# Kernel tuning notes

Hardware: AMD Instinct MI355X
Metric: run time of the kernel (lower is better)

Reference implementation:

```python
import jax, jax.numpy as jnp
import numpy as np

INPUT_DIM = 1024
OUT_DIM = 1024
ORDER = 4
EXPANSION_POINT = 0.0


def setup_inputs() -> dict:
    key = jax.random.key(0)
    k_x, k_c = jax.random.split(key)
    x = jax.random.normal(k_x, (8192, INPUT_DIM), dtype=jnp.float32)
    coeffs = jax.random.normal(k_c, (OUT_DIM, INPUT_DIM, ORDER), dtype=jnp.float32) * 0.01
    bias = jnp.zeros((1, OUT_DIM), dtype=jnp.float32)
    return {"x": x, "coeffs": coeffs, "bias": bias}


def reference(x, coeffs, bias):
    # x: [..., input_dim] -> flatten leading dims
    outshape = x.shape[:-1] + (OUT_DIM,)
    xf = x.reshape(-1, INPUT_DIM)
    x_shifted = xf - EXPANSION_POINT
    # powers P[n, i, k] = x_shifted^k, k = 0..order-1 (0**0 == 1, matching torch)
    powers = jnp.power(x_shifted[:, :, None], jnp.arange(ORDER, dtype=x.dtype))
    # y[n, o] = sum_{i,k} P[n,i,k] * coeffs[o,i,k]  -- single GEMM-like contraction
    y = jnp.einsum('nik,oik->no', powers, coeffs)
    y = y + bias
    return y.reshape(outshape)
```

## Files before the change

### kernel.cpp

```cpp
#include <hip/hip_runtime.h>
#include <stdint.h>

#define IN_DIM 1024
#define OUT_DIM 1024
#define NROWS 8192
#define KD 3072

#define BM 128
#define BN 128
#define BK 64
#define NT (KD / BK)

typedef __bf16 bf16x8 __attribute__((ext_vector_type(8)));
typedef float f32x4 __attribute__((ext_vector_type(4)));
typedef unsigned short us8 __attribute__((ext_vector_type(8)));
typedef unsigned int u32;

#define AS1 __attribute__((address_space(1)))
#define AS3 __attribute__((address_space(3)))

__device__ __forceinline__ unsigned short f2bf(float f) {
    u32 u = __builtin_bit_cast(u32, f);
    u32 r = (u + 0x7fffu + ((u >> 16) & 1u)) >> 16;
    return (unsigned short)r;
}

__device__ __forceinline__ bf16x8 ld8(const unsigned short* p) {
    return __builtin_bit_cast(bf16x8, *reinterpret_cast<const us8*>(p));
}

__global__ __launch_bounds__(256) void prep_coeffs(const float* __restrict__ c,
                                                   const float* __restrict__ bias,
                                                   unsigned short* __restrict__ B,
                                                   float* __restrict__ bias2) {
    const int o = blockIdx.x;
    const float4* row = reinterpret_cast<const float4*>(c + (size_t)o * (IN_DIM * 4));
    unsigned short* Bo = B + (size_t)o * KD;
    float s = 0.f;
    for (int i = threadIdx.x; i < IN_DIM; i += 256) {
        float4 v = row[i];
        s += v.x;
        Bo[i]        = f2bf(v.y);
        Bo[1024 + i] = f2bf(v.z);
        Bo[2048 + i] = f2bf(v.w);
    }
#pragma unroll
    for (int off = 32; off; off >>= 1) s += __shfl_down(s, off);
    __shared__ float red[4];
    if ((threadIdx.x & 63) == 0) red[threadIdx.x >> 6] = s;
    __syncthreads();
    if (threadIdx.x == 0) bias2[o] = bias[o] + red[0] + red[1] + red[2] + red[3];
}

__global__ __launch_bounds__(256) void prep_powers(const float* __restrict__ x,
                                                   unsigned short* __restrict__ A) {
    int t = blockIdx.x * blockDim.x + threadIdx.x;
    int n = t >> 8;
    int i4 = (t & 255) * 4;
    float4 v = reinterpret_cast<const float4*>(x)[t];
    unsigned short* An = A + (size_t)n * KD + i4;
    float xs[4] = {v.x, v.y, v.z, v.w};
    unsigned short b1[4], b2[4], b3[4];
#pragma unroll
    for (int j = 0; j < 4; ++j) {
        float x1 = xs[j], x2 = x1 * x1, x3 = x2 * x1;
        b1[j] = f2bf(x1); b2[j] = f2bf(x2); b3[j] = f2bf(x3);
    }
    ushort4 p1 = {b1[0], b1[1], b1[2], b1[3]};
    ushort4 p2 = {b2[0], b2[1], b2[2], b2[3]};
    ushort4 p3 = {b3[0], b3[1], b3[2], b3[3]};
    *reinterpret_cast<ushort4*>(An)        = p1;
    *reinterpret_cast<ushort4*>(An + 1024) = p2;
    *reinterpret_cast<ushort4*>(An + 2048) = p3;
}

__global__ __launch_bounds__(256, 2) void taylor_gemm(
    const unsigned short* __restrict__ A,
    const unsigned short* __restrict__ B,
    const float* __restrict__ bias2,
    float* __restrict__ C) {
    __shared__ alignas(16) unsigned short sA[2][BM * BK];
    __shared__ alignas(16) unsigned short sB[2][BN * BK];

    const int tid = threadIdx.x;
    const int lane = tid & 63;
    const int wid = tid >> 6;
    const int wr = wid >> 1;
    const int wc = wid & 1;
    const int gx = blockIdx.x, gy = blockIdx.y;

    const char* Ab = (const char*)A;
    const char* Bb = (const char*)B;
    const int cs = ((lane & 7) ^ (lane >> 3)) * 8;
    size_t aSrc[4], bSrc[4];
    int dstOff[4];
#pragma unroll
    for (int u = 0; u < 4; ++u) {
        int row = u * 32 + wid * 8 + (lane >> 3);
        aSrc[u] = ((size_t)(gx * BM + row) * KD + cs) * 2;
        bSrc[u] = ((size_t)(gy * BN + row) * KD + cs) * 2;
        dstOff[u] = row * BK - (lane >> 3) * BK;
    }

    auto stage_all = [&](int d, int kt) {
        size_t koff = (size_t)kt * (BK * 2);
#pragma unroll
        for (int u = 0; u < 4; ++u)
            __builtin_amdgcn_global_load_lds(
                (const AS1 void*)(Ab + aSrc[u] + koff),
                (AS3 void*)(&sA[d][dstOff[u]]), 16, 0, 0);
#pragma unroll
        for (int u = 0; u < 4; ++u)
            __builtin_amdgcn_global_load_lds(
                (const AS1 void*)(Bb + bSrc[u] + koff),
                (AS3 void*)(&sB[d][dstOff[u]]), 16, 0, 0);
    };

    int aSw[2], bSw[2];
#pragma unroll
    for (int ks = 0; ks < 2; ++ks) {
        int sw = ((ks * 4 + (lane >> 4)) ^ (lane & 7)) * 8;
        aSw[ks] = (wr * 64 + (lane & 15)) * BK + sw;
        bSw[ks] = (wc * 64 + (lane & 15)) * BK + sw;
    }

    f32x4 acc[4][4] = {};

    stage_all(0, 0);
    asm volatile("s_waitcnt vmcnt(0)" ::: "memory");
    __builtin_amdgcn_s_barrier();
    __builtin_amdgcn_sched_barrier(0);

    for (int kt = 0; kt < NT; ++kt) {
        const int d = kt & 1;
        const unsigned short* sAc = &sA[d][0];
        const unsigned short* sBc = &sB[d][0];

        bf16x8 af[4][2], bf[4][2];
#pragma unroll
        for (int m = 0; m < 4; ++m)
#pragma unroll
            for (int ks = 0; ks < 2; ++ks)
                af[m][ks] = ld8(&sAc[aSw[ks] + m * 16 * BK]);
#pragma unroll
        for (int n = 0; n < 4; ++n)
#pragma unroll
            for (int ks = 0; ks < 2; ++ks)
                bf[n][ks] = ld8(&sBc[bSw[ks] + n * 16 * BK]);

        if (kt + 1 < NT) stage_all(d ^ 1, kt + 1);

#pragma unroll
        for (int m = 0; m < 4; ++m)
#pragma unroll
            for (int n = 0; n < 4; ++n)
#pragma unroll
                for (int ks = 0; ks < 2; ++ks)
                    acc[m][n] = __builtin_amdgcn_mfma_f32_16x16x32_bf16(
                        af[m][ks], bf[n][ks], acc[m][n], 0, 0, 0);

        asm volatile("s_waitcnt vmcnt(0)" ::: "memory");
        __builtin_amdgcn_s_barrier();
        __builtin_amdgcn_sched_barrier(0);
    }

    const int colBase = gy * BN + wc * 64 + (lane & 15);
    const int rowBase = gx * BM + wr * 64 + (lane >> 4) * 4;
#pragma unroll
    for (int n = 0; n < 4; ++n) {
        int col = colBase + n * 16;
        float bv = bias2[col];
#pragma unroll
        for (int m = 0; m < 4; ++m) {
            int row = rowBase + m * 16;
#pragma unroll
            for (int r = 0; r < 4; ++r)
                C[(size_t)(row + r) * OUT_DIM + col] = acc[m][n][r] + bv;
        }
    }
}

__global__ void taylor_naive(const float* __restrict__ x, const float* __restrict__ coeffs,
                             const float* __restrict__ bias, float* __restrict__ out) {
    int n = blockIdx.x;
    __shared__ float P[IN_DIM * 4];
    for (int i = threadIdx.x; i < IN_DIM; i += blockDim.x) {
        float xv = x[(size_t)n * IN_DIM + i];
        P[i * 4 + 0] = 1.f;
        P[i * 4 + 1] = xv;
        P[i * 4 + 2] = xv * xv;
        P[i * 4 + 3] = xv * xv * xv;
    }
    __syncthreads();
    for (int o = threadIdx.x; o < OUT_DIM; o += blockDim.x) {
        float s = bias[o];
        const float* c = coeffs + (size_t)o * (IN_DIM * 4);
        for (int i = 0; i < IN_DIM; ++i) {
            float4 cv = *reinterpret_cast<const float4*>(c + i * 4);
            s += cv.x * P[i * 4 + 0] + cv.y * P[i * 4 + 1] +
                 cv.z * P[i * 4 + 2] + cv.w * P[i * 4 + 3];
        }
        out[(size_t)n * OUT_DIM + o] = s;
    }
}

extern "C" void kernel_launch(void* const* d_in, const int* in_sizes, int n_in,
                              void* d_out, int out_size, void* d_ws, size_t ws_size,
                              hipStream_t stream) {
    const float* x = (const float*)d_in[0];
    const float* coeffs = (const float*)d_in[1];
    const float* bias = (const float*)d_in[2];
    float* out = (float*)d_out;

    const size_t needA = (size_t)NROWS * KD * 2;
    const size_t needB = (size_t)OUT_DIM * KD * 2;
    const size_t needBias = OUT_DIM * sizeof(float);

    if (ws_size >= needA + needB + needBias) {
        unsigned short* A = (unsigned short*)d_ws;
        unsigned short* B = (unsigned short*)((char*)d_ws + needA);
        float* bias2 = (float*)((char*)d_ws + needA + needB);
        prep_coeffs<<<OUT_DIM, 256, 0, stream>>>(coeffs, bias, B, bias2);
        prep_powers<<<(NROWS * IN_DIM / 4) / 256, 256, 0, stream>>>(x, A);
        dim3 grid(NROWS / BM, OUT_DIM / BN);
        taylor_gemm<<<grid, 256, 0, stream>>>(A, B, bias2, out);
    } else {
        taylor_naive<<<NROWS, 256, 0, stream>>>(x, coeffs, bias, out);
    }
}
```

Measured before the change: 76.86 us.

## Load A fragments straight from global into double-buffered registers, keep B in LDS

The GEMM now skips LDS staging for the A (powers) operand. Each wave reads its A MFMA fragments directly from global memory into two register buffers that alternate between k-steps, while B is still staged into double-buffered LDS through global_load_lds. The full vmcnt(0) wait is relaxed to vmcnt(8), so the next k-tile's A loads can stay in flight while the current tile's MFMAs run. This removes LDS writes and reads for A and halves LDS use. In exchange, the two waves sharing the same rows fetch the same A data twice, the per-lane global reads are strided, and register pressure rises.

New measurement: 134.4 us. +74.9%, slower.

```diff
diff --git a/kernel.cpp b/kernel.cpp
--- a/kernel.cpp
+++ b/kernel.cpp
@@ -79,7 +79,6 @@
     const unsigned short* __restrict__ B,
     const float* __restrict__ bias2,
     float* __restrict__ C) {
-    __shared__ alignas(16) unsigned short sA[2][BM * BK];
     __shared__ alignas(16) unsigned short sB[2][BN * BK];
 
     const int tid = threadIdx.x;
@@ -89,26 +88,19 @@
     const int wc = wid & 1;
     const int gx = blockIdx.x, gy = blockIdx.y;
 
-    const char* Ab = (const char*)A;
     const char* Bb = (const char*)B;
     const int cs = ((lane & 7) ^ (lane >> 3)) * 8;
-    size_t aSrc[4], bSrc[4];
+    size_t bSrc[4];
     int dstOff[4];
 #pragma unroll
     for (int u = 0; u < 4; ++u) {
         int row = u * 32 + wid * 8 + (lane >> 3);
-        aSrc[u] = ((size_t)(gx * BM + row) * KD + cs) * 2;
         bSrc[u] = ((size_t)(gy * BN + row) * KD + cs) * 2;
-        dstOff[u] = row * BK - (lane >> 3) * BK;
-    }
-
-    auto stage_all = [&](int d, int kt) {
+        dstOff[u] = (u * 32 + wid * 8) * BK;
+    }
+
+    auto stage_B = [&](int d, int kt) {
         size_t koff = (size_t)kt * (BK * 2);
-#pragma unroll
-        for (int u = 0; u < 4; ++u)
-            __builtin_amdgcn_global_load_lds(
-                (const AS1 void*)(Ab + aSrc[u] + koff),
-                (AS3 void*)(&sA[d][dstOff[u]]), 16, 0, 0);
 #pragma unroll
         for (int u = 0; u < 4; ++u)
             __builtin_amdgcn_global_load_lds(
@@ -116,53 +108,65 @@
                 (AS3 void*)(&sB[d][dstOff[u]]), 16, 0, 0);
     };
 
-    int aSw[2], bSw[2];
-#pragma unroll
-    for (int ks = 0; ks < 2; ++ks) {
-        int sw = ((ks * 4 + (lane >> 4)) ^ (lane & 7)) * 8;
-        aSw[ks] = (wr * 64 + (lane & 15)) * BK + sw;
-        bSw[ks] = (wc * 64 + (lane & 15)) * BK + sw;
-    }
-
+    int bSw[2];
+#pragma unroll
+    for (int ks = 0; ks < 2; ++ks)
+        bSw[ks] = (wc * 64 + (lane & 15)) * BK
+                + (((ks * 4 + (lane >> 4)) ^ (lane & 7)) * 8);
+
+    const unsigned short* aPtr[4];
+#pragma unroll
+    for (int m = 0; m < 4; ++m)
+        aPtr[m] = A + (size_t)(gx * BM + wr * 64 + m * 16 + (lane & 15)) * KD
+                    + ((lane >> 4) * 8);
+
+    bf16x8 aR0[4][2], aR1[4][2];
     f32x4 acc[4][4] = {};
 
-    stage_all(0, 0);
-    asm volatile("s_waitcnt vmcnt(0)" ::: "memory");
-    __builtin_amdgcn_s_barrier();
+    auto load_A = [&](bf16x8 (&ar)[4][2], int kt) {
+#pragma unroll
+        for (int m = 0; m < 4; ++m)
+#pragma unroll
+            for (int ks = 0; ks < 2; ++ks)
+                ar[m][ks] = ld8(aPtr[m] + kt * BK + ks * 32);
+    };
+
+    stage_B(0, 0);
     __builtin_amdgcn_sched_barrier(0);
-
-    for (int kt = 0; kt < NT; ++kt) {
-        const int d = kt & 1;
-        const unsigned short* sAc = &sA[d][0];
-        const unsigned short* sBc = &sB[d][0];
-
-        bf16x8 af[4][2], bf[4][2];
-#pragma unroll
-        for (int m = 0; m < 4; ++m)
-#pragma unroll
-            for (int ks = 0; ks < 2; ++ks)
-                af[m][ks] = ld8(&sAc[aSw[ks] + m * 16 * BK]);
-#pragma unroll
-        for (int n = 0; n < 4; ++n)
-#pragma unroll
-            for (int ks = 0; ks < 2; ++ks)
-                bf[n][ks] = ld8(&sBc[bSw[ks] + n * 16 * BK]);
-
-        if (kt + 1 < NT) stage_all(d ^ 1, kt + 1);
-
-#pragma unroll
-        for (int m = 0; m < 4; ++m)
-#pragma unroll
-            for (int n = 0; n < 4; ++n)
-#pragma unroll
-                for (int ks = 0; ks < 2; ++ks)
-                    acc[m][n] = __builtin_amdgcn_mfma_f32_16x16x32_bf16(
-                        af[m][ks], bf[n][ks], acc[m][n], 0, 0, 0);
-
-        asm volatile("s_waitcnt vmcnt(0)" ::: "memory");
-        __builtin_amdgcn_s_barrier();
-        __builtin_amdgcn_sched_barrier(0);
-    }
+    load_A(aR0, 0);
+
+#define TAYLOR_ITER(kt, CUR, NXT)                                             \
+    {                                                                         \
+        asm volatile("s_waitcnt vmcnt(8)" ::: "memory");                      \
+        __builtin_amdgcn_s_barrier();                                         \
+        __builtin_amdgcn_sched_barrier(0);                                    \
+        if ((kt) + 1 < NT) {                                                  \
+            stage_B(((kt) + 1) & 1, (kt) + 1);                                \
+            __builtin_amdgcn_sched_barrier(0);                                \
+            load_A(NXT, (kt) + 1);                                            \
+        }                                                                     \
+        const unsigned short* sBc = &sB[(kt) & 1][0];                         \
+        bf16x8 bf[4][2];                                                      \
+        _Pragma("unroll")                                                     \
+        for (int n = 0; n < 4; ++n)                                           \
+            _Pragma("unroll")                                                 \
+            for (int ks = 0; ks < 2; ++ks)                                    \
+                bf[n][ks] = ld8(&sBc[bSw[ks] + n * 16 * BK]);                 \
+        _Pragma("unroll")                                                     \
+        for (int m = 0; m < 4; ++m)                                           \
+            _Pragma("unroll")                                                 \
+            for (int n = 0; n < 4; ++n)                                       \
+                _Pragma("unroll")                                             \
+                for (int ks = 0; ks < 2; ++ks)                                \
+                    acc[m][n] = __builtin_amdgcn_mfma_f32_16x16x32_bf16(      \
+                        CUR[m][ks], bf[n][ks], acc[m][n], 0, 0, 0);           \
+    }
+
+    for (int kt = 0; kt < NT; kt += 2) {
+        TAYLOR_ITER(kt,     aR0, aR1);
+        TAYLOR_ITER(kt + 1, aR1, aR0);
+    }
+#undef TAYLOR_ITER
 
     const int colBase = gy * BN + wc * 64 + (lane & 15);
     const int rowBase = gx * BM + wr * 64 + (lane >> 4) * 4;
```

## Enlarge GEMM M-tile to 256 and use triple-buffered LDS prefetch

Applied to the files above, without the earlier changes.

Doubles the block tile in M so each wave computes a 128x64 sub-tile, which raises MFMA work per LDS fragment load and halves re-reads of B from global memory. The shared-memory staging moves from two buffers to three, and loads are issued two k-steps ahead with a partial vmcnt wait, so global-to-LDS copies overlap with compute. In exchange, occupancy drops to one block per CU, with 144KB of LDS and twice the accumulator registers, and the grid shrinks to 256 blocks.

After: 125.5 us. 1.63x slower.

```diff
diff --git a/kernel.cpp b/kernel.cpp
--- a/kernel.cpp
+++ b/kernel.cpp
@@ -6,7 +6,7 @@
 #define NROWS 8192
 #define KD 3072
 
-#define BM 128
+#define BM 256
 #define BN 128
 #define BK 64
 #define NT (KD / BK)
@@ -74,13 +74,13 @@
     *reinterpret_cast<ushort4*>(An + 2048) = p3;
 }
 
-__global__ __launch_bounds__(256, 2) void taylor_gemm(
+__global__ __launch_bounds__(256, 1) void taylor_gemm(
     const unsigned short* __restrict__ A,
     const unsigned short* __restrict__ B,
     const float* __restrict__ bias2,
     float* __restrict__ C) {
-    __shared__ alignas(16) unsigned short sA[2][BM * BK];
-    __shared__ alignas(16) unsigned short sB[2][BN * BK];
+    __shared__ alignas(16) unsigned short sA[3][BM * BK];
+    __shared__ alignas(16) unsigned short sB[3][BN * BK];
 
     const int tid = threadIdx.x;
     const int lane = tid & 63;
@@ -92,86 +92,90 @@
     const char* Ab = (const char*)A;
     const char* Bb = (const char*)B;
     const int cs = ((lane & 7) ^ (lane >> 3)) * 8;
-    size_t aSrc[4], bSrc[4];
-    int dstOff[4];
+    size_t aSrc[8], bSrc[4];
+    int aDst[8], bDst[4];
+#pragma unroll
+    for (int u = 0; u < 8; ++u) {
+        int rb = wid * 64 + u * 8;
+        aSrc[u] = ((size_t)(gx * BM + rb + (lane >> 3)) * KD + cs) * 2;
+        aDst[u] = rb * BK;
+    }
 #pragma unroll
     for (int u = 0; u < 4; ++u) {
-        int row = u * 32 + wid * 8 + (lane >> 3);
-        aSrc[u] = ((size_t)(gx * BM + row) * KD + cs) * 2;
-        bSrc[u] = ((size_t)(gy * BN + row) * KD + cs) * 2;
-        dstOff[u] = row * BK - (lane >> 3) * BK;
-    }
-
-    auto stage_all = [&](int d, int kt) {
+        int rb = wid * 32 + u * 8;
+        bSrc[u] = ((size_t)(gy * BN + rb + (lane >> 3)) * KD + cs) * 2;
+        bDst[u] = rb * BK;
+    }
+
+    auto stage_all = [&](int b, int kt) {
         size_t koff = (size_t)kt * (BK * 2);
 #pragma unroll
-        for (int u = 0; u < 4; ++u)
+        for (int u = 0; u < 8; ++u)
             __builtin_amdgcn_global_load_lds(
                 (const AS1 void*)(Ab + aSrc[u] + koff),
-                (AS3 void*)(&sA[d][dstOff[u]]), 16, 0, 0);
+                (AS3 void*)(&sA[b][aDst[u]]), 16, 0, 0);
 #pragma unroll
         for (int u = 0; u < 4; ++u)
             __builtin_amdgcn_global_load_lds(
                 (const AS1 void*)(Bb + bSrc[u] + koff),
-                (AS3 void*)(&sB[d][dstOff[u]]), 16, 0, 0);
+                (AS3 void*)(&sB[b][bDst[u]]), 16, 0, 0);
     };
 
     int aSw[2], bSw[2];
 #pragma unroll
     for (int ks = 0; ks < 2; ++ks) {
         int sw = ((ks * 4 + (lane >> 4)) ^ (lane & 7)) * 8;
-        aSw[ks] = (wr * 64 + (lane & 15)) * BK + sw;
+        aSw[ks] = (wr * 128 + (lane & 15)) * BK + sw;
         bSw[ks] = (wc * 64 + (lane & 15)) * BK + sw;
     }
 
-    f32x4 acc[4][4] = {};
+    f32x4 acc[8][4] = {};
 
     stage_all(0, 0);
-    asm volatile("s_waitcnt vmcnt(0)" ::: "memory");
-    __builtin_amdgcn_s_barrier();
-    __builtin_amdgcn_sched_barrier(0);
+    stage_all(1, 1);
 
     for (int kt = 0; kt < NT; ++kt) {
-        const int d = kt & 1;
-        const unsigned short* sAc = &sA[d][0];
-        const unsigned short* sBc = &sB[d][0];
-
-        bf16x8 af[4][2], bf[4][2];
-#pragma unroll
-        for (int m = 0; m < 4; ++m)
+        const int cb = kt % 3;
+        if (kt < NT - 1) asm volatile("s_waitcnt vmcnt(12)" ::: "memory");
+        else             asm volatile("s_waitcnt vmcnt(0)" ::: "memory");
+        __builtin_amdgcn_s_barrier();
+        __builtin_amdgcn_sched_barrier(0);
+
+        if (kt + 2 < NT) stage_all((kt + 2) % 3, kt + 2);
+
+        const unsigned short* sAc = &sA[cb][0];
+        const unsigned short* sBc = &sB[cb][0];
+
+        bf16x8 bf[4][2], af[8][2];
+#pragma unroll
+        for (int n = 0; n < 4; ++n)
+#pragma unroll
+            for (int ks = 0; ks < 2; ++ks)
+                bf[n][ks] = ld8(&sBc[bSw[ks] + n * 16 * BK]);
+#pragma unroll
+        for (int m = 0; m < 8; ++m)
 #pragma unroll
             for (int ks = 0; ks < 2; ++ks)
                 af[m][ks] = ld8(&sAc[aSw[ks] + m * 16 * BK]);
-#pragma unroll
-        for (int n = 0; n < 4; ++n)
-#pragma unroll
-            for (int ks = 0; ks < 2; ++ks)
-                bf[n][ks] = ld8(&sBc[bSw[ks] + n * 16 * BK]);
-
-        if (kt + 1 < NT) stage_all(d ^ 1, kt + 1);
-
-#pragma unroll
-        for (int m = 0; m < 4; ++m)
+
+#pragma unroll
+        for (int m = 0; m < 8; ++m)
 #pragma unroll
             for (int n = 0; n < 4; ++n)
 #pragma unroll
                 for (int ks = 0; ks < 2; ++ks)
                     acc[m][n] = __builtin_amdgcn_mfma_f32_16x16x32_bf16(
                         af[m][ks], bf[n][ks], acc[m][n], 0, 0, 0);
-
-        asm volatile("s_waitcnt vmcnt(0)" ::: "memory");
-        __builtin_amdgcn_s_barrier();
-        __builtin_amdgcn_sched_barrier(0);
     }
 
     const int colBase = gy * BN + wc * 64 + (lane & 15);
-    const int rowBase = gx * BM + wr * 64 + (lane >> 4) * 4;
+    const int rowBase = gx * BM + wr * 128 + (lane >> 4) * 4;
 #pragma unroll
     for (int n = 0; n < 4; ++n) {
         int col = colBase + n * 16;
         float bv = bias2[col];
 #pragma unroll
-        for (int m = 0; m < 4; ++m) {
+        for (int m = 0; m < 8; ++m) {
             int row = rowBase + m * 16;
 #pragma unroll
             for (int r = 0; r < 4; ++r)
```
